# Kernel tuning notes

Measured on AMD Instinct MI355X. Metric: run time of the kernel, lower is better.

Reference implementation:

```python
import jax, jax.numpy as jnp
import numpy as np

B, L, D, H = 2, 2048, 1024, 16
HD = D // H

def setup_inputs() -> dict:
    key = jax.random.key(0)
    ks = jax.random.split(key, 9)
    s = 1.0 / np.sqrt(D)
    return {
        "query": jax.random.normal(ks[0], (B, L, D), dtype=jnp.float32),
        "Wq": jax.random.uniform(ks[1], (D, D), jnp.float32, -s, s),
        "bq": jax.random.uniform(ks[2], (D,), jnp.float32, -s, s),
        "Wk": jax.random.uniform(ks[3], (D, D), jnp.float32, -s, s),
        "bk": jax.random.uniform(ks[4], (D,), jnp.float32, -s, s),
        "Wv": jax.random.uniform(ks[5], (D, D), jnp.float32, -s, s),
        "bv": jax.random.uniform(ks[6], (D,), jnp.float32, -s, s),
        "Wo": jax.random.uniform(ks[7], (D, D), jnp.float32, -s, s),
        "bo": jax.random.uniform(ks[8], (D,), jnp.float32, -s, s),
    }

def reference(query, Wq, bq, Wk, bk, Wv, bv, Wo, bo):
    # self-attention: key_value = query. Linear: x @ W.T + b (torch convention)
    scale = HD ** -0.5
    q = (query @ Wq.T + bq).reshape(B, L, H, HD).transpose(0, 2, 1, 3)  # (B,H,L,hd)
    k = (query @ Wk.T + bk).reshape(B, L, H, HD).transpose(0, 2, 1, 3)
    v = (query @ Wv.T + bv).reshape(B, L, H, HD).transpose(0, 2, 1, 3)
    logits = jnp.einsum('bhqd,bhkd->bhqk', q, k) * scale  # (B,H,Lq,Lk)
    attn = jax.nn.softmax(logits, axis=-1)
    out = jnp.einsum('bhqk,bhkd->bhqd', attn, v)
    out = out.transpose(0, 2, 1, 3).reshape(B, L, D)
    return out @ Wo.T + bo
```

## Files before the change

kernel.cpp:

```cpp
#include <hip/hip_runtime.h>

#define Bc 2
#define Lc 2048
#define Dc 1024
#define Hc 16
#define HDc 64
#define LOG2E 1.44269504088896340736f

typedef __bf16 bf16x8 __attribute__((ext_vector_type(8)));
typedef __bf16 bf16x2 __attribute__((ext_vector_type(2)));
typedef float f32x4 __attribute__((ext_vector_type(4)));
typedef unsigned short u16;
typedef unsigned int u32;
typedef unsigned long long u64;

__device__ __forceinline__ u16 f2bf(float x) {
    union { float f; u32 u; } c; c.f = x;
    u32 u = c.u + 0x7fffu + ((c.u >> 16) & 1u);
    return (u16)(u >> 16);
}

__device__ __forceinline__ u32 pkbf(float a, float b) {
#if __has_builtin(__builtin_amdgcn_cvt_pk_bf16_f32)
    union { bf16x2 v; u32 u; } c;
    c.v = __builtin_amdgcn_cvt_pk_bf16_f32(a, b);
    return c.u;
#else
    return (u32)f2bf(a) | ((u32)f2bf(b) << 16);
#endif
}

__device__ __forceinline__ float fexp2(float x) {
#if __has_builtin(__builtin_amdgcn_exp2f)
    return __builtin_amdgcn_exp2f(x);
#else
    return exp2f(x);
#endif
}

__device__ __forceinline__ void g2l16(const void* g, void* l) {
    __builtin_amdgcn_global_load_lds(
        (const __attribute__((address_space(1))) void*)g,
        (__attribute__((address_space(3))) void*)l, 16, 0, 0);
}

__global__ __launch_bounds__(256) void cast_bf16(
    const float* __restrict__ x,
    const float* __restrict__ wq, const float* __restrict__ wk,
    const float* __restrict__ wv, const float* __restrict__ wo,
    u16* __restrict__ xb, u16* __restrict__ wqb, u16* __restrict__ wkb,
    u16* __restrict__ wvb, u16* __restrict__ wob)
{
    const int i = blockIdx.x * 256 + threadIdx.x;
    const float* s; u16* d; int off;
    if (i < 1048576) { s = x; d = xb; off = i; }
    else {
        const int j = i - 1048576;
        const int sel = j >> 18;
        off = j & 262143;
        s = sel == 0 ? wq : sel == 1 ? wk : sel == 2 ? wv : wo;
        d = sel == 0 ? wqb : sel == 1 ? wkb : sel == 2 ? wvb : wob;
    }
    const float4 f = ((const float4*)s)[off];
    ushort4 o;
    o.x = f2bf(f.x); o.y = f2bf(f.y); o.z = f2bf(f.z); o.w = f2bf(f.w);
    ((ushort4*)d)[off] = o;
}

__device__ __forceinline__ void gemm128_body(
    const u16* __restrict__ A, const u16* __restrict__ Bm,
    int row0, int col0, int K,
    f32x4 (&acc)[4][4], u16* As, u16* Bs)
{
    const int tid  = threadIdx.x;
    const int w    = tid >> 6;
    const int lane = tid & 63;
    const int l15  = lane & 15, quad = lane >> 4;
    const int srow = lane >> 3;
    const int sxor = ((lane & 7) ^ srow) << 3;
    const int wm   = (w & 1) << 6, wn = (w >> 1) << 6;
    const int l7   = l15 & 7;

    for (int k0 = 0; k0 < K; k0 += 64) {
        __syncthreads();
#pragma unroll
        for (int s = 0; s < 4; ++s) {
            const int rb = w * 32 + s * 8;
            g2l16(&A [(size_t)(row0 + rb + srow) * K + k0 + sxor], &As[rb * 64]);
            g2l16(&Bm[(size_t)(col0 + rb + srow) * K + k0 + sxor], &Bs[rb * 64]);
        }
        __syncthreads();

#pragma unroll
        for (int kk = 0; kk < 2; ++kk) {
            bf16x8 af[4], bf[4];
#pragma unroll
            for (int i = 0; i < 4; ++i)
                af[i] = *(const bf16x8*)&As[(wm + i * 16 + l15) * 64 +
                                            (((kk * 4 + quad) ^ l7) << 3)];
#pragma unroll
            for (int j = 0; j < 4; ++j)
                bf[j] = *(const bf16x8*)&Bs[(wn + j * 16 + l15) * 64 +
                                            (((kk * 4 + quad) ^ l7) << 3)];
#pragma unroll
            for (int i = 0; i < 4; ++i)
#pragma unroll
                for (int j = 0; j < 4; ++j)
                    acc[i][j] = __builtin_amdgcn_mfma_f32_16x16x32_bf16(
                        af[i], bf[j], acc[i][j], 0, 0, 0);
        }
    }
}

__device__ __forceinline__ void gemm_o_body(
    const u16* __restrict__ A, const u16* __restrict__ Bm,
    int row0, int col0, int K,
    f32x4 (&acc)[4][2], u16* As, u16* Bs)
{
    const int tid  = threadIdx.x;
    const int w    = tid >> 6;
    const int lane = tid & 63;
    const int l15  = lane & 15, quad = lane >> 4;
    const int srow = lane >> 3;
    const int sxor = ((lane & 7) ^ srow) << 3;
    const int wm   = (w & 1) << 6, wn = (w >> 1) << 5;
    const int l7   = l15 & 7;

    for (int k0 = 0; k0 < K; k0 += 64) {
        __syncthreads();
#pragma unroll
        for (int s = 0; s < 6; ++s) {
            const int c = w * 6 + s;
            if (c < 16) {
                const int rb = c * 8;
                g2l16(&A [(size_t)(row0 + rb + srow) * K + k0 + sxor], &As[rb * 64]);
            } else {
                const int rb = (c - 16) * 8;
                g2l16(&Bm[(size_t)(col0 + rb + srow) * K + k0 + sxor], &Bs[rb * 64]);
            }
        }
        __syncthreads();

#pragma unroll
        for (int kk = 0; kk < 2; ++kk) {
            bf16x8 af[4], bf[2];
#pragma unroll
            for (int i = 0; i < 4; ++i)
                af[i] = *(const bf16x8*)&As[(wm + i * 16 + l15) * 64 +
                                            (((kk * 4 + quad) ^ l7) << 3)];
#pragma unroll
            for (int j = 0; j < 2; ++j)
                bf[j] = *(const bf16x8*)&Bs[(wn + j * 16 + l15) * 64 +
                                            (((kk * 4 + quad) ^ l7) << 3)];
#pragma unroll
            for (int i = 0; i < 4; ++i)
#pragma unroll
                for (int j = 0; j < 2; ++j)
                    acc[i][j] = __builtin_amdgcn_mfma_f32_16x16x32_bf16(
                        af[i], bf[j], acc[i][j], 0, 0, 0);
        }
    }
}

__global__ __launch_bounds__(256) void gemm_qkv_bf16(
    const u16* __restrict__ Xb,
    const u16* __restrict__ Wqb, const u16* __restrict__ Wkb, const u16* __restrict__ Wvb,
    const float* __restrict__ bq, const float* __restrict__ bk, const float* __restrict__ bv,
    u16* __restrict__ qo, u16* __restrict__ ko, u16* __restrict__ vto)
{
    __shared__ __attribute__((aligned(16))) u16 As[128 * 64];
    __shared__ __attribute__((aligned(16))) u16 Bs[128 * 64];

    const int z = blockIdx.z;
    const int tid = threadIdx.x;
    const int w = tid >> 6, lane = tid & 63;
    const int l15 = lane & 15, quad = lane >> 4;
    const int wm = (w & 1) << 6, wn = (w >> 1) << 6;

    f32x4 acc[4][4];
#pragma unroll
    for (int i = 0; i < 4; ++i)
#pragma unroll
        for (int j = 0; j < 4; ++j)
#pragma unroll
            for (int r = 0; r < 4; ++r) acc[i][j][r] = 0.0f;

    if (z == 2) {
        const int row0 = blockIdx.x << 7;
        const int col0 = blockIdx.y << 7;
        gemm128_body(Xb, Wvb, row0, col0, Dc, acc, As, Bs);

        const int b = row0 >> 11;
#pragma unroll
        for (int j = 0; j < 4; ++j) {
            const int n = col0 + wn + j * 16 + l15;
            const float bj = bv[n];
            const int hh = n >> 6, hd = n & 63;
            u16* vbase = vto + (((size_t)(b * Hc + hh) * HDc + hd) << 11);
#pragma unroll
            for (int i = 0; i < 4; ++i) {
                const int l = (row0 + wm + i * 16 + quad * 4) & (Lc - 1);
                uint2 pr;
                pr.x = pkbf(acc[i][j][0] + bj, acc[i][j][1] + bj);
                pr.y = pkbf(acc[i][j][2] + bj, acc[i][j][3] + bj);
                *(uint2*)&vbase[l] = pr;
            }
        }
        return;
    }

    const u16*   W    = z == 0 ? Wqb : Wkb;
    const float* bias = z == 0 ? bq  : bk;
    u16*         outp = z == 0 ? qo  : ko;
    const int row0 = blockIdx.y << 7;
    const int col0 = blockIdx.x << 7;
    gemm128_body(W, Xb, row0, col0, Dc, acc, As, Bs);

    const float qs = z == 0 ? 0.125f * LOG2E : 1.0f;
    const int h = (row0 + wm) >> 6;
    float4 b4[4];
#pragma unroll
    for (int i = 0; i < 4; ++i)
        b4[i] = *(const float4*)&bias[row0 + wm + i * 16 + quad * 4];

#pragma unroll
    for (int j = 0; j < 4; ++j) {
        const int tok = col0 + wn + j * 16 + l15;
        const int bb = tok >> 11, ll = tok & (Lc - 1);
        u16* obase = outp + (((size_t)(bb * Hc + h) * Lc + ll) << 6);
#pragma unroll
        for (int i = 0; i < 4; ++i) {
            uint2 pr;
            pr.x = pkbf((acc[i][j][0] + b4[i].x) * qs, (acc[i][j][1] + b4[i].y) * qs);
            pr.y = pkbf((acc[i][j][2] + b4[i].z) * qs, (acc[i][j][3] + b4[i].w) * qs);
            *(uint2*)&obase[i * 16 + quad * 4] = pr;
        }
    }
}

__global__ __launch_bounds__(512) void attn_mfma(
    const u16* __restrict__ q, const u16* __restrict__ k,
    const u16* __restrict__ vt, u16* __restrict__ out)
{
    __shared__ __attribute__((aligned(16))) u16 smem[17408];
    u16* Ks0 = smem;
    u16* Vs0 = smem + 8192;

    const int tid = threadIdx.x;
    const int w = tid >> 6, lane = tid & 63;
    const int l15 = lane & 15, quad = lane >> 4;
    const int bh = blockIdx.x & 31;
    const int qt = blockIdx.x >> 5;
    const int h  = bh & (Hc - 1);
    const int b  = bh >> 4;
    const int l0 = qt << 7;
    const int wq = w & 3;
    const int hf = w >> 2;

    const size_t bhs = (size_t)(b * Hc + h) * (Lc * HDc);
    const u16* qb = q  + bhs;
    const u16* kb = k  + bhs;
    const u16* vb = vt + bhs;

    bf16x8 qf[2][2];
#pragma unroll
    for (int mt = 0; mt < 2; ++mt) {
        const size_t row = (size_t)(l0 + wq * 32 + mt * 16 + l15) * HDc;
        qf[mt][0] = *(const bf16x8*)&qb[row + quad * 8];
        qf[mt][1] = *(const bf16x8*)&qb[row + 32 + quad * 8];
    }

    const int srow  = lane >> 2;
    const int sunit = lane & 3;
    const int gd = (l15 >> 1) & 3;

    f32x4 oacc[2][4];
    float l_i[2] = {0.0f, 0.0f};
#pragma unroll
    for (int mt = 0; mt < 2; ++mt)
#pragma unroll
        for (int dt = 0; dt < 4; ++dt)
#pragma unroll
            for (int r = 0; r < 4; ++r) oacc[mt][dt][r] = 0.0f;

    for (int kt = 0; kt < Lc; kt += 128) {
        __syncthreads();
#pragma unroll
        for (int i = 0; i < 4; ++i) {
            const int c = w * 4 + i;
            if (c < 16) {
                const int p = c >> 3, g = c & 7;
                const int row = g * 16 + srow;
                g2l16(&kb[(size_t)(kt + row) * HDc + p * 32 +
                          ((sunit ^ ((row >> 1) & 3)) << 3)],
                      &Ks0[p * 4096 + g * 512]);
            } else {
                const int cc = c - 16;
                const int cp = cc >> 2, g = cc & 3;
                const int row = g * 16 + srow;
                g2l16(&vb[(size_t)row * Lc + kt + cp * 32 +
                          ((sunit ^ ((row >> 1) & 3)) << 3)],
                      &Vs0[cp * 2048 + g * 512]);
            }
        }
        __syncthreads();

        f32x4 st[2][4];
        __builtin_amdgcn_s_setprio(1);
#pragma unroll
        for (int t = 0; t < 4; ++t) {
            const int j   = (hf * 4 + t) * 16 + l15;
            const int off = j * 32 + ((quad ^ gd) << 3);
            const bf16x8 kf0 = *(const bf16x8*)&Ks0[off];
            const bf16x8 kf1 = *(const bf16x8*)&Ks0[4096 + off];
#pragma unroll
            for (int mt = 0; mt < 2; ++mt) {
                f32x4 z = {0.0f, 0.0f, 0.0f, 0.0f};
                z = __builtin_amdgcn_mfma_f32_16x16x32_bf16(kf0, qf[mt][0], z, 0, 0, 0);
                st[mt][t] = __builtin_amdgcn_mfma_f32_16x16x32_bf16(kf1, qf[mt][1], z, 0, 0, 0);
            }
        }
        __builtin_amdgcn_s_setprio(0);

        u32 pk[2][4][2];
#pragma unroll
        for (int mt = 0; mt < 2; ++mt) {
            f32x4 s4 = {0.0f, 0.0f, 0.0f, 0.0f};
#pragma unroll
            for (int t = 0; t < 4; ++t) {
                f32x4 p;
#pragma unroll
                for (int r = 0; r < 4; ++r) p[r] = fexp2(st[mt][t][r]);
                s4 += p;
                pk[mt][t][0] = pkbf(p[0], p[1]);
                pk[mt][t][1] = pkbf(p[2], p[3]);
            }
            l_i[mt] += s4[0] + s4[1] + s4[2] + s4[3];
        }

        __builtin_amdgcn_s_setprio(1);
#pragma unroll
        for (int cpl = 0; cpl < 2; ++cpl) {
            const int cp = hf * 2 + cpl;
            union { bf16x8 v; u32 uw[4]; } pf0, pf1;
            pf0.uw[0] = pk[0][2 * cpl][0];     pf0.uw[1] = pk[0][2 * cpl][1];
            pf0.uw[2] = pk[0][2 * cpl + 1][0]; pf0.uw[3] = pk[0][2 * cpl + 1][1];
            pf1.uw[0] = pk[1][2 * cpl][0];     pf1.uw[1] = pk[1][2 * cpl][1];
            pf1.uw[2] = pk[1][2 * cpl + 1][0]; pf1.uw[3] = pk[1][2 * cpl + 1][1];
#pragma unroll
            for (int dt = 0; dt < 4; ++dt) {
                const int base = cp * 2048 + (dt * 16 + l15) * 32 + ((quad & 1) << 2);
                union { bf16x8 v; u64 d[2]; } vf;
                vf.d[0] = *(const u64*)&Vs0[base + (((quad >> 1) ^ gd) << 3)];
                vf.d[1] = *(const u64*)&Vs0[base + (((2 + (quad >> 1)) ^ gd) << 3)];
                oacc[0][dt] = __builtin_amdgcn_mfma_f32_16x16x32_bf16(
                    vf.v, pf0.v, oacc[0][dt], 0, 0, 0);
                oacc[1][dt] = __builtin_amdgcn_mfma_f32_16x16x32_bf16(
                    vf.v, pf1.v, oacc[1][dt], 0, 0, 0);
            }
        }
        __builtin_amdgcn_s_setprio(0);
    }

    __syncthreads();
    float* co = (float*)smem;
    float* cl = (float*)(smem + 16384);
    if (w >= 4) {
        const int base = (w - 4) * 64 + lane;
#pragma unroll
        for (int mt = 0; mt < 2; ++mt)
#pragma unroll
            for (int dt = 0; dt < 4; ++dt)
#pragma unroll
                for (int r = 0; r < 4; ++r)
                    co[(mt * 16 + dt * 4 + r) * 256 + base] = oacc[mt][dt][r];
        cl[base]       = l_i[0];
        cl[256 + base] = l_i[1];
    }
    __syncthreads();
    if (w >= 4) return;
    {
        const int base = w * 64 + lane;
#pragma unroll
        for (int mt = 0; mt < 2; ++mt)
#pragma unroll
            for (int dt = 0; dt < 4; ++dt)
#pragma unroll
                for (int r = 0; r < 4; ++r)
                    oacc[mt][dt][r] += co[(mt * 16 + dt * 4 + r) * 256 + base];
        l_i[0] += cl[base];
        l_i[1] += cl[256 + base];
    }

#pragma unroll
    for (int mt = 0; mt < 2; ++mt) {
        float l = l_i[mt];
        l += __shfl_xor(l, 16);
        l += __shfl_xor(l, 32);
        const float inv = 1.0f / l;
        const int lrow = l0 + wq * 32 + mt * 16 + l15;
        u16* ob = out + ((size_t)(b * Lc + lrow)) * Dc + h * HDc;
#pragma unroll
        for (int dt = 0; dt < 4; ++dt) {
            uint2 pr;
            pr.x = pkbf(oacc[mt][dt][0] * inv, oacc[mt][dt][1] * inv);
            pr.y = pkbf(oacc[mt][dt][2] * inv, oacc[mt][dt][3] * inv);
            *(uint2*)&ob[dt * 16 + quad * 4] = pr;
        }
    }
}

__global__ __launch_bounds__(256) void gemm_o_bf16(
    const u16* __restrict__ Ab, const u16* __restrict__ Wob,
    const float* __restrict__ bo, float* __restrict__ out)
{
    __shared__ __attribute__((aligned(16))) u16 As[128 * 64];
    __shared__ __attribute__((aligned(16))) u16 Bs[64 * 64];
    const int row0 = blockIdx.y << 7;
    const int col0 = blockIdx.x << 6;

    f32x4 acc[4][2];
#pragma unroll
    for (int i = 0; i < 4; ++i)
#pragma unroll
        for (int j = 0; j < 2; ++j)
#pragma unroll
            for (int r = 0; r < 4; ++r) acc[i][j][r] = 0.0f;

    gemm_o_body(Wob, Ab, row0, col0, Dc, acc, As, Bs);

    const int tid = threadIdx.x;
    const int w = tid >> 6, lane = tid & 63;
    const int l15 = lane & 15, quad = lane >> 4;
    const int wm = (w & 1) << 6, wn = (w >> 1) << 5;

    float4 b4[4];
#pragma unroll
    for (int i = 0; i < 4; ++i)
        b4[i] = *(const float4*)&bo[row0 + wm + i * 16 + quad * 4];

#pragma unroll
    for (int j = 0; j < 2; ++j) {
        const int tok = col0 + wn + j * 16 + l15;
        float* obase = out + (size_t)tok * Dc + row0 + wm;
#pragma unroll
        for (int i = 0; i < 4; ++i) {
            float4 o;
            o.x = acc[i][j][0] + b4[i].x; o.y = acc[i][j][1] + b4[i].y;
            o.z = acc[i][j][2] + b4[i].z; o.w = acc[i][j][3] + b4[i].w;
            *(float4*)&obase[i * 16 + quad * 4] = o;
        }
    }
}

extern "C" void kernel_launch(void* const* d_in, const int* in_sizes, int n_in,
                              void* d_out, int out_size, void* d_ws, size_t ws_size,
                              hipStream_t stream)
{
    const float* query = (const float*)d_in[0];
    const float* Wq = (const float*)d_in[1];
    const float* bq = (const float*)d_in[2];
    const float* Wk = (const float*)d_in[3];
    const float* bk = (const float*)d_in[4];
    const float* Wv = (const float*)d_in[5];
    const float* bv = (const float*)d_in[6];
    const float* Wo = (const float*)d_in[7];
    const float* bo = (const float*)d_in[8];

    u16* ws = (u16*)d_ws;
    const size_t nX = (size_t)Bc * Lc * Dc;
    const size_t nW = (size_t)Dc * Dc;
    u16* xb  = ws;
    u16* wqb = xb + nX;
    u16* wkb = wqb + nW;
    u16* wvb = wkb + nW;
    u16* wob = wvb + nW;
    u16* q_w = wob + nW;
    u16* k_w = q_w + nX;
    u16* vt_w = k_w + nX;
    u16* a_w = vt_w + nX;

    cast_bf16<<<dim3(8192), 256, 0, stream>>>(query, Wq, Wk, Wv, Wo,
                                              xb, wqb, wkb, wvb, wob);
    gemm_qkv_bf16<<<dim3(32, 8, 3), 256, 0, stream>>>(xb, wqb, wkb, wvb,
                                                      bq, bk, bv, q_w, k_w, vt_w);
    attn_mfma<<<dim3(512), 512, 0, stream>>>(q_w, k_w, vt_w, a_w);
    gemm_o_bf16<<<dim3(64, 8), 256, 0, stream>>>(a_w, wob, bo, (float*)d_out);
}
```

Before: 197.1 us.

## Load K and V fragments directly from global memory instead of LDS staging

The attention kernel no longer stages K and V tiles into shared memory with two barriers per iteration. Each wave reads its K and V MFMA fragments straight from global memory, relying on L1/L2 caching to serve the reuse across the four query waves that share each key tile. This removes the per-iteration block synchronisation and LDS traffic, but adds redundant global loads and exposes global-memory latency directly to the MFMA loop. Dropping the final barrier before the shared-memory reduction is safe because LDS is no longer written inside the loop.

```diff
diff --git a/kernel.cpp b/kernel.cpp
--- a/kernel.cpp
+++ b/kernel.cpp
@@ -243,8 +243,6 @@
     const u16* __restrict__ vt, u16* __restrict__ out)
 {
     __shared__ __attribute__((aligned(16))) u16 smem[17408];
-    u16* Ks0 = smem;
-    u16* Vs0 = smem + 8192;
 
     const int tid = threadIdx.x;
     const int w = tid >> 6, lane = tid & 63;
@@ -270,10 +268,6 @@
         qf[mt][1] = *(const bf16x8*)&qb[row + 32 + quad * 8];
     }
 
-    const int srow  = lane >> 2;
-    const int sunit = lane & 3;
-    const int gd = (l15 >> 1) & 3;
-
     f32x4 oacc[2][4];
     float l_i[2] = {0.0f, 0.0f};
 #pragma unroll
@@ -283,36 +277,17 @@
 #pragma unroll
             for (int r = 0; r < 4; ++r) oacc[mt][dt][r] = 0.0f;
 
+    const int voff = ((quad >> 1) << 3) + ((quad & 1) << 2);
+
     for (int kt = 0; kt < Lc; kt += 128) {
-        __syncthreads();
-#pragma unroll
-        for (int i = 0; i < 4; ++i) {
-            const int c = w * 4 + i;
-            if (c < 16) {
-                const int p = c >> 3, g = c & 7;
-                const int row = g * 16 + srow;
-                g2l16(&kb[(size_t)(kt + row) * HDc + p * 32 +
-                          ((sunit ^ ((row >> 1) & 3)) << 3)],
-                      &Ks0[p * 4096 + g * 512]);
-            } else {
-                const int cc = c - 16;
-                const int cp = cc >> 2, g = cc & 3;
-                const int row = g * 16 + srow;
-                g2l16(&vb[(size_t)row * Lc + kt + cp * 32 +
-                          ((sunit ^ ((row >> 1) & 3)) << 3)],
-                      &Vs0[cp * 2048 + g * 512]);
-            }
-        }
-        __syncthreads();
-
         f32x4 st[2][4];
         __builtin_amdgcn_s_setprio(1);
 #pragma unroll
         for (int t = 0; t < 4; ++t) {
-            const int j   = (hf * 4 + t) * 16 + l15;
-            const int off = j * 32 + ((quad ^ gd) << 3);
-            const bf16x8 kf0 = *(const bf16x8*)&Ks0[off];
-            const bf16x8 kf1 = *(const bf16x8*)&Ks0[4096 + off];
+            const int j = (hf * 4 + t) * 16 + l15;
+            const u16* krow = &kb[(size_t)(kt + j) * HDc + quad * 8];
+            const bf16x8 kf0 = *(const bf16x8*)krow;
+            const bf16x8 kf1 = *(const bf16x8*)(krow + 32);
 #pragma unroll
             for (int mt = 0; mt < 2; ++mt) {
                 f32x4 z = {0.0f, 0.0f, 0.0f, 0.0f};
@@ -349,10 +324,11 @@
             pf1.uw[2] = pk[1][2 * cpl + 1][0]; pf1.uw[3] = pk[1][2 * cpl + 1][1];
 #pragma unroll
             for (int dt = 0; dt < 4; ++dt) {
-                const int base = cp * 2048 + (dt * 16 + l15) * 32 + ((quad & 1) << 2);
-                union { bf16x8 v; u64 d[2]; } vf;
-                vf.d[0] = *(const u64*)&Vs0[base + (((quad >> 1) ^ gd) << 3)];
-                vf.d[1] = *(const u64*)&Vs0[base + (((2 + (quad >> 1)) ^ gd) << 3)];
+                const int d = dt * 16 + l15;
+                const u16* vrow = &vb[(size_t)d * Lc + kt + cp * 32 + voff];
+                union { bf16x8 v; u64 dd[2]; } vf;
+                vf.dd[0] = *(const u64*)vrow;
+                vf.dd[1] = *(const u64*)(vrow + 16);
                 oacc[0][dt] = __builtin_amdgcn_mfma_f32_16x16x32_bf16(
                     vf.v, pf0.v, oacc[0][dt], 0, 0, 0);
                 oacc[1][dt] = __builtin_amdgcn_mfma_f32_16x16x32_bf16(
@@ -362,7 +338,6 @@
         __builtin_amdgcn_s_setprio(0);
     }
 
-    __syncthreads();
     float* co = (float*)smem;
     float* cl = (float*)(smem + 16384);
     if (w >= 4) {
```

Measured after the change: 322.9 us. +63.8%, slower.

## Split attention KV tile across four wave groups and halve query tile per block

Applied to the files above, without the earlier changes.

The attention kernel now gives each block 64 query rows instead of 128, with 2 waves along queries and 4 waves splitting the key/value tile four ways. The grid doubles to 1024 blocks. A two-stage shared-memory reduction then combines the partial outputs and row sums. This is meant to raise parallelism and occupancy across CUs. The cost is that K/V tiles are loaded twice as often per query, and the reduction adds an extra barrier stage.

```diff
diff --git a/kernel.cpp b/kernel.cpp
--- a/kernel.cpp
+++ b/kernel.cpp
@@ -253,9 +253,9 @@
     const int qt = blockIdx.x >> 5;
     const int h  = bh & (Hc - 1);
     const int b  = bh >> 4;
-    const int l0 = qt << 7;
-    const int wq = w & 3;
-    const int hf = w >> 2;
+    const int l0 = qt << 6;
+    const int wq = w & 1;
+    const int hf = w >> 1;
 
     const size_t bhs = (size_t)(b * Hc + h) * (Lc * HDc);
     const u16* qb = q  + bhs;
@@ -305,11 +305,11 @@
         }
         __syncthreads();
 
-        f32x4 st[2][4];
+        f32x4 st[2][2];
         __builtin_amdgcn_s_setprio(1);
 #pragma unroll
-        for (int t = 0; t < 4; ++t) {
-            const int j   = (hf * 4 + t) * 16 + l15;
+        for (int t = 0; t < 2; ++t) {
+            const int j   = (hf * 2 + t) * 16 + l15;
             const int off = j * 32 + ((quad ^ gd) << 3);
             const bf16x8 kf0 = *(const bf16x8*)&Ks0[off];
             const bf16x8 kf1 = *(const bf16x8*)&Ks0[4096 + off];
@@ -322,12 +322,12 @@
         }
         __builtin_amdgcn_s_setprio(0);
 
-        u32 pk[2][4][2];
+        u32 pk[2][2][2];
 #pragma unroll
         for (int mt = 0; mt < 2; ++mt) {
             f32x4 s4 = {0.0f, 0.0f, 0.0f, 0.0f};
 #pragma unroll
-            for (int t = 0; t < 4; ++t) {
+            for (int t = 0; t < 2; ++t) {
                 f32x4 p;
 #pragma unroll
                 for (int r = 0; r < 4; ++r) p[r] = fexp2(st[mt][t][r]);
@@ -339,14 +339,13 @@
         }
 
         __builtin_amdgcn_s_setprio(1);
-#pragma unroll
-        for (int cpl = 0; cpl < 2; ++cpl) {
-            const int cp = hf * 2 + cpl;
+        {
+            const int cp = hf;
             union { bf16x8 v; u32 uw[4]; } pf0, pf1;
-            pf0.uw[0] = pk[0][2 * cpl][0];     pf0.uw[1] = pk[0][2 * cpl][1];
-            pf0.uw[2] = pk[0][2 * cpl + 1][0]; pf0.uw[3] = pk[0][2 * cpl + 1][1];
-            pf1.uw[0] = pk[1][2 * cpl][0];     pf1.uw[1] = pk[1][2 * cpl][1];
-            pf1.uw[2] = pk[1][2 * cpl + 1][0]; pf1.uw[3] = pk[1][2 * cpl + 1][1];
+            pf0.uw[0] = pk[0][0][0]; pf0.uw[1] = pk[0][0][1];
+            pf0.uw[2] = pk[0][1][0]; pf0.uw[3] = pk[0][1][1];
+            pf1.uw[0] = pk[1][0][0]; pf1.uw[1] = pk[1][0][1];
+            pf1.uw[2] = pk[1][1][0]; pf1.uw[3] = pk[1][1][1];
 #pragma unroll
             for (int dt = 0; dt < 4; ++dt) {
                 const int base = cp * 2048 + (dt * 16 + l15) * 32 + ((quad & 1) << 2);
@@ -378,8 +377,7 @@
         cl[256 + base] = l_i[1];
     }
     __syncthreads();
-    if (w >= 4) return;
-    {
+    if (w < 4) {
         const int base = w * 64 + lane;
 #pragma unroll
         for (int mt = 0; mt < 2; ++mt)
@@ -390,6 +388,33 @@
                     oacc[mt][dt][r] += co[(mt * 16 + dt * 4 + r) * 256 + base];
         l_i[0] += cl[base];
         l_i[1] += cl[256 + base];
+    }
+    __syncthreads();
+    if (w == 2 || w == 3) {
+        const int base = (w - 2) * 64 + lane;
+#pragma unroll
+        for (int mt = 0; mt < 2; ++mt)
+#pragma unroll
+            for (int dt = 0; dt < 4; ++dt)
+#pragma unroll
+                for (int r = 0; r < 4; ++r)
+                    co[(mt * 16 + dt * 4 + r) * 128 + base] = oacc[mt][dt][r];
+        cl[base]       = l_i[0];
+        cl[128 + base] = l_i[1];
+    }
+    __syncthreads();
+    if (w >= 2) return;
+    {
+        const int base = w * 64 + lane;
+#pragma unroll
+        for (int mt = 0; mt < 2; ++mt)
+#pragma unroll
+            for (int dt = 0; dt < 4; ++dt)
+#pragma unroll
+                for (int r = 0; r < 4; ++r)
+                    oacc[mt][dt][r] += co[(mt * 16 + dt * 4 + r) * 128 + base];
+        l_i[0] += cl[base];
+        l_i[1] += cl[128 + base];
     }
 
 #pragma unroll
@@ -484,6 +509,6 @@
                                               xb, wqb, wkb, wvb, wob);
     gemm_qkv_bf16<<<dim3(32, 8, 3), 256, 0, stream>>>(xb, wqb, wkb, wvb,
                                                       bq, bk, bv, q_w, k_w, vt_w);
-    attn_mfma<<<dim3(512), 512, 0, stream>>>(q_w, k_w, vt_w, a_w);
+    attn_mfma<<<dim3(1024), 512, 0, stream>>>(q_w, k_w, vt_w, a_w);
     gemm_o_bf16<<<dim3(64, 8), 256, 0, stream>>>(a_w, wob, bo, (float*)d_out);
 }
```

After: 205.1 us. 4.1% more time.
